# Kernel optimization log

Hardware: AMD Instinct MI355X
Metric: run time of the kernel (lower is better)

Reference implementation:

```python
import jax, jax.numpy as jnp
import numpy as np

B, Q, K, QS, KS, H, DV = 16, 128, 512, 256, 256, 128, 256


def setup_inputs() -> dict:
    key = jax.random.key(0)
    ks = jax.random.split(key, 7)
    return {
        "queries": jax.random.normal(ks[0], (B, Q, QS), dtype=jnp.float32),
        "keys": jax.random.normal(ks[1], (B, K, KS), dtype=jnp.float32),
        "values": jax.random.normal(ks[2], (B, K, DV), dtype=jnp.float32),
        "valid_lens": jax.random.randint(ks[3], (B,), 1, K + 1),
        # Linear weights (no bias); stored as [in, hidden] so x @ W == nn.Linear
        "W_q": jax.random.normal(ks[4], (QS, H), dtype=jnp.float32) / np.float32(np.sqrt(QS)),
        "W_k": jax.random.normal(ks[5], (KS, H), dtype=jnp.float32) / np.float32(np.sqrt(KS)),
        "w_v": jax.random.normal(ks[6], (H,), dtype=jnp.float32) / np.float32(np.sqrt(H)),
    }


def reference(queries, keys, values, valid_lens, W_q, W_k, w_v):
    # Projections
    q = jnp.einsum('bqd,dh->bqh', queries, W_q)   # [B,Q,H]
    k = jnp.einsum('bkd,dh->bkh', keys, W_k)      # [B,K,H]
    # Additive (Bahdanau) score: tanh(q + k) . w_v  -> [B,Q,K]
    feats = jnp.tanh(q[:, :, None, :] + k[:, None, :, :])  # [B,Q,K,H] big intermediate
    scores = jnp.einsum('bqkh,h->bqk', feats, w_v)
    # masked softmax over keys: positions >= valid_len get -1e6 (as in torch ref)
    mask = jnp.arange(K)[None, None, :] < valid_lens[:, None, None]  # [B,1,K] bcast
    scores = jnp.where(mask, scores, jnp.float32(-1e6))
    attn = jax.nn.softmax(scores, axis=-1)        # [B,Q,K]
    # dropout p=0.0 -> identity
    return jnp.einsum('bqk,bkd->bqd', attn, values)  # [B,Q,DV]
```

## Files before the change

### kernel.cpp

```cpp
#include <hip/hip_runtime.h>
#include <hip/hip_bf16.h>

#define NB 16
#define NQ 128
#define NK 512
#define DIN 256
#define NH 128
#define NDV 256

#define CSC 2.8853900817779268f

__global__ __launch_bounds__(256) void proj_both_kernel(
    const float* __restrict__ Q, const float* __restrict__ K,
    const float* __restrict__ Wq, const float* __restrict__ Wk,
    float* __restrict__ QP, float* __restrict__ KPT)
{
    __shared__ float Xl[32 * DIN];
    const int tid = threadIdx.x;
    int blk = blockIdx.x;
    const float* X; const float* W;
    int b, r0, isq;
    if (blk < 64) { isq = 1; b = blk >> 2; r0 = (blk & 3) * 32;
                    X = Q + ((size_t)b * NQ + r0) * DIN; W = Wq; }
    else { blk -= 64; isq = 0; b = blk >> 4; r0 = (blk & 15) * 32;
           X = K + ((size_t)b * NK + r0) * DIN; W = Wk; }

    {
        const float4* Xg = (const float4*)X;
        float4* Xs = (float4*)Xl;
        #pragma unroll
        for (int i = 0; i < 8; ++i) Xs[tid + 256 * i] = Xg[tid + 256 * i];
    }
    __syncthreads();

    const int h4 = tid & 31;
    const int rg = tid >> 5;
    const float4* Wv = (const float4*)W;

    float4 acc[4];
    #pragma unroll
    for (int r = 0; r < 4; ++r) { acc[r].x = 0.f; acc[r].y = 0.f; acc[r].z = 0.f; acc[r].w = 0.f; }

    float4 w0 = Wv[0 * 32 + h4], w1 = Wv[1 * 32 + h4], w2 = Wv[2 * 32 + h4], w3 = Wv[3 * 32 + h4];
    float4 n0 = Wv[4 * 32 + h4], n1 = Wv[5 * 32 + h4], n2 = Wv[6 * 32 + h4], n3 = Wv[7 * 32 + h4];
    for (int d = 0; d < DIN; d += 4) {
        const int dp = (d + 8 < DIN) ? d + 8 : 0;
        float4 m0 = Wv[(dp + 0) * 32 + h4];
        float4 m1 = Wv[(dp + 1) * 32 + h4];
        float4 m2 = Wv[(dp + 2) * 32 + h4];
        float4 m3 = Wv[(dp + 3) * 32 + h4];
        #pragma unroll
        for (int r = 0; r < 4; ++r) {
            float4 x = *(const float4*)&Xl[(rg * 4 + r) * DIN + d];
            acc[r].x += x.x * w0.x + x.y * w1.x + x.z * w2.x + x.w * w3.x;
            acc[r].y += x.x * w0.y + x.y * w1.y + x.z * w2.y + x.w * w3.y;
            acc[r].z += x.x * w0.z + x.y * w1.z + x.z * w2.z + x.w * w3.z;
            acc[r].w += x.x * w0.w + x.y * w1.w + x.z * w2.w + x.w * w3.w;
        }
        w0 = n0; w1 = n1; w2 = n2; w3 = n3;
        n0 = m0; n1 = m1; n2 = m2; n3 = m3;
    }
    #pragma unroll
    for (int r = 0; r < 4; ++r) {
        acc[r].x *= CSC; acc[r].y *= CSC; acc[r].z *= CSC; acc[r].w *= CSC;
    }

    if (isq) {
        #pragma unroll
        for (int r = 0; r < 4; ++r)
            *(float4*)&QP[((size_t)b * NQ + r0 + rg * 4 + r) * NH + 4 * h4] = acc[r];
    } else {
        float* T = Xl;
        __syncthreads();
        #pragma unroll
        for (int r = 0; r < 4; ++r) {
            T[(4 * h4 + 0) * 36 + rg * 4 + r] = acc[r].x;
            T[(4 * h4 + 1) * 36 + rg * 4 + r] = acc[r].y;
            T[(4 * h4 + 2) * 36 + rg * 4 + r] = acc[r].z;
            T[(4 * h4 + 3) * 36 + rg * 4 + r] = acc[r].w;
        }
        __syncthreads();
        #pragma unroll
        for (int i = 0; i < 4; ++i) {
            const int idx = tid + 256 * i;
            const int h = idx >> 3, c8 = idx & 7;
            float4 v = *(const float4*)&T[h * 36 + c8 * 4];
            *(float4*)&KPT[((size_t)b * NH + h) * NK + r0 + c8 * 4] = v;
        }
    }
}

__global__ __launch_bounds__(512) void attn_fused_kernel(
    const float* __restrict__ QP, const float* __restrict__ KPT,
    const float* __restrict__ wv, const int* __restrict__ vlen,
    const float* __restrict__ V, float* __restrict__ OUT)
{
    __shared__ float qcl[4 * NH];
    __shared__ float wvl[NH];
    __shared__ float sc[4][NK];
    __shared__ float part[4][4][NDV];
    const int tid = threadIdx.x;
    const int b  = blockIdx.x & 15;
    const int q0 = (blockIdx.x >> 4) * 4;

    qcl[tid] = QP[((size_t)b * NQ + q0) * NH + tid];
    if (tid < NH) wvl[tid] = -2.0f * wv[tid];
    __syncthreads();

    int vl = vlen[b];
    vl = vl < 1 ? 1 : (vl > NK ? NK : vl);

    {
        const float* kb = KPT + (size_t)b * NH * NK + tid;
        float a0 = 0.f, a1 = 0.f, a2 = 0.f, a3 = 0.f;
        #pragma unroll 4
        for (int h = 0; h < NH; ++h) {
            float kv = kb[(size_t)h * NK];
            float wq = wvl[h];
            float e0 = __builtin_amdgcn_exp2f(qcl[0 * NH + h] + kv);
            float e1 = __builtin_amdgcn_exp2f(qcl[1 * NH + h] + kv);
            float e2 = __builtin_amdgcn_exp2f(qcl[2 * NH + h] + kv);
            float e3 = __builtin_amdgcn_exp2f(qcl[3 * NH + h] + kv);
            a0 += wq * __builtin_amdgcn_rcpf(e0 + 1.0f);
            a1 += wq * __builtin_amdgcn_rcpf(e1 + 1.0f);
            a2 += wq * __builtin_amdgcn_rcpf(e2 + 1.0f);
            a3 += wq * __builtin_amdgcn_rcpf(e3 + 1.0f);
        }
        const bool vld = (tid < vl);
        sc[0][tid] = vld ? a0 : -1e6f;
        sc[1][tid] = vld ? a1 : -1e6f;
        sc[2][tid] = vld ? a2 : -1e6f;
        sc[3][tid] = vld ? a3 : -1e6f;
    }
    __syncthreads();

    const int w = tid >> 6, lane = tid & 63;
    if (w < 4) {
        float vals[8];
        float m = -3.0e38f;
        #pragma unroll
        for (int i = 0; i < 8; ++i) { vals[i] = sc[w][lane + 64 * i]; m = fmaxf(m, vals[i]); }
        #pragma unroll
        for (int off = 32; off; off >>= 1) m = fmaxf(m, __shfl_xor(m, off, 64));
        float s = 0.f;
        #pragma unroll
        for (int i = 0; i < 8; ++i) {
            vals[i] = __builtin_amdgcn_exp2f((vals[i] - m) * 1.4426950408889634f);
            s += vals[i];
        }
        #pragma unroll
        for (int off = 32; off; off >>= 1) s += __shfl_xor(s, off, 64);
        const float invs = 1.0f / s;
        #pragma unroll
        for (int i = 0; i < 8; ++i) sc[w][lane + 64 * i] = vals[i] * invs;
    }
    __syncthreads();

    float4 o[4];
    #pragma unroll
    for (int r = 0; r < 4; ++r) { o[r].x = 0.f; o[r].y = 0.f; o[r].z = 0.f; o[r].w = 0.f; }
    {
        const float* vb = V + (size_t)b * NK * NDV + lane * 4;
        const int kb0 = w * 64;
        #pragma unroll 4
        for (int kk = 0; kk < 64; ++kk) {
            const int k = kb0 + kk;
            float4 v4 = *(const float4*)(vb + (size_t)k * NDV);
            float p0 = sc[0][k], p1 = sc[1][k], p2 = sc[2][k], p3 = sc[3][k];
            o[0].x += p0 * v4.x; o[0].y += p0 * v4.y; o[0].z += p0 * v4.z; o[0].w += p0 * v4.w;
            o[1].x += p1 * v4.x; o[1].y += p1 * v4.y; o[1].z += p1 * v4.z; o[1].w += p1 * v4.w;
            o[2].x += p2 * v4.x; o[2].y += p2 * v4.y; o[2].z += p2 * v4.z; o[2].w += p2 * v4.w;
            o[3].x += p3 * v4.x; o[3].y += p3 * v4.y; o[3].z += p3 * v4.z; o[3].w += p3 * v4.w;
        }
    }
    if (w >= 4) {
        #pragma unroll
        for (int r = 0; r < 4; ++r) *(float4*)&part[w - 4][r][lane * 4] = o[r];
    }
    __syncthreads();
    if (w < 4) {
        #pragma unroll
        for (int r = 0; r < 4; ++r) {
            float4 t = *(const float4*)&part[w][r][lane * 4];
            o[r].x += t.x; o[r].y += t.y; o[r].z += t.z; o[r].w += t.w;
            *(float4*)&part[w][r][lane * 4] = o[r];
        }
    }
    __syncthreads();
    if (tid < 256) {
        const int r = tid >> 6, d4 = tid & 63;
        float4 s = {0.f, 0.f, 0.f, 0.f};
        #pragma unroll
        for (int p = 0; p < 4; ++p) {
            float4 q = *(const float4*)&part[p][r][d4 * 4];
            s.x += q.x; s.y += q.y; s.z += q.z; s.w += q.w;
        }
        *(float4*)&OUT[((size_t)b * NQ + q0 + r) * NDV + d4 * 4] = s;
    }
}

extern "C" void kernel_launch(void* const* d_in, const int* in_sizes, int n_in,
                              void* d_out, int out_size, void* d_ws, size_t ws_size,
                              hipStream_t stream) {
    const float* queries = (const float*)d_in[0];
    const float* keys    = (const float*)d_in[1];
    const float* values  = (const float*)d_in[2];
    const int*   vlen    = (const int*)d_in[3];
    const float* Wq      = (const float*)d_in[4];
    const float* Wk      = (const float*)d_in[5];
    const float* wv      = (const float*)d_in[6];
    float* out           = (float*)d_out;

    float* qp  = (float*)d_ws;
    float* kpt = qp + (size_t)NB * NQ * NH;

    proj_both_kernel<<<64 + 256, 256, 0, stream>>>(queries, keys, Wq, Wk, qp, kpt);
    attn_fused_kernel<<<NB * 32, 512, 0, stream>>>(qp, kpt, wv, vlen, values, out);
}
```

Measured before the change: 132.1 us.

## Factor tanh exponent into per-row exp products and skip masked keys

The projection kernel now stores exp2(c*q) and exp2(c*k) rather than the scaled projections. The inner score loop therefore computes 1/(eq*ek+1) with one FMA and one reciprocal, dropping the per-element exp. Key projection blocks, score computation and value accumulation are also skipped for keys beyond valid_len, and q values are stored interleaved for float4 LDS reads. Risks include overflow or underflow of the separate exponentials for large projections, which could turn into inf*0 NaNs, and skipping padded keys relies on masked weights being exactly zero after softmax.

```diff
diff --git a/kernel.cpp b/kernel.cpp
--- a/kernel.cpp
+++ b/kernel.cpp
@@ -13,7 +13,8 @@
 __global__ __launch_bounds__(256) void proj_both_kernel(
     const float* __restrict__ Q, const float* __restrict__ K,
     const float* __restrict__ Wq, const float* __restrict__ Wk,
-    float* __restrict__ QP, float* __restrict__ KPT)
+    const int* __restrict__ vlen,
+    float* __restrict__ EQ, float* __restrict__ EKT)
 {
     __shared__ float Xl[32 * DIN];
     const int tid = threadIdx.x;
@@ -23,7 +24,10 @@
     if (blk < 64) { isq = 1; b = blk >> 2; r0 = (blk & 3) * 32;
                     X = Q + ((size_t)b * NQ + r0) * DIN; W = Wq; }
     else { blk -= 64; isq = 0; b = blk >> 4; r0 = (blk & 15) * 32;
-           X = K + ((size_t)b * NK + r0) * DIN; W = Wk; }
+           X = K + ((size_t)b * NK + r0) * DIN; W = Wk;
+           int vl = vlen[b]; vl = vl < 1 ? 1 : (vl > NK ? NK : vl);
+           if (r0 >= vl) return;
+    }
 
     {
         const float4* Xg = (const float4*)X;
@@ -62,13 +66,16 @@
     }
     #pragma unroll
     for (int r = 0; r < 4; ++r) {
-        acc[r].x *= CSC; acc[r].y *= CSC; acc[r].z *= CSC; acc[r].w *= CSC;
+        acc[r].x = __builtin_amdgcn_exp2f(CSC * acc[r].x);
+        acc[r].y = __builtin_amdgcn_exp2f(CSC * acc[r].y);
+        acc[r].z = __builtin_amdgcn_exp2f(CSC * acc[r].z);
+        acc[r].w = __builtin_amdgcn_exp2f(CSC * acc[r].w);
     }
 
     if (isq) {
         #pragma unroll
         for (int r = 0; r < 4; ++r)
-            *(float4*)&QP[((size_t)b * NQ + r0 + rg * 4 + r) * NH + 4 * h4] = acc[r];
+            *(float4*)&EQ[((size_t)b * NQ + r0 + rg * 4 + r) * NH + 4 * h4] = acc[r];
     } else {
         float* T = Xl;
         __syncthreads();
@@ -85,17 +92,17 @@
             const int idx = tid + 256 * i;
             const int h = idx >> 3, c8 = idx & 7;
             float4 v = *(const float4*)&T[h * 36 + c8 * 4];
-            *(float4*)&KPT[((size_t)b * NH + h) * NK + r0 + c8 * 4] = v;
+            *(float4*)&EKT[((size_t)b * NH + h) * NK + r0 + c8 * 4] = v;
         }
     }
 }
 
 __global__ __launch_bounds__(512) void attn_fused_kernel(
-    const float* __restrict__ QP, const float* __restrict__ KPT,
+    const float* __restrict__ EQ, const float* __restrict__ EKT,
     const float* __restrict__ wv, const int* __restrict__ vlen,
     const float* __restrict__ V, float* __restrict__ OUT)
 {
-    __shared__ float qcl[4 * NH];
+    __shared__ float eq4[NH * 4];
     __shared__ float wvl[NH];
     __shared__ float sc[4][NK];
     __shared__ float part[4][4][NDV];
@@ -103,7 +110,10 @@
     const int b  = blockIdx.x & 15;
     const int q0 = (blockIdx.x >> 4) * 4;
 
-    qcl[tid] = QP[((size_t)b * NQ + q0) * NH + tid];
+    {
+        const int r = tid >> 7, h = tid & 127;
+        eq4[h * 4 + r] = EQ[((size_t)b * NQ + q0 + r) * NH + h];
+    }
     if (tid < NH) wvl[tid] = -2.0f * wv[tid];
     __syncthreads();
 
@@ -111,22 +121,21 @@
     vl = vl < 1 ? 1 : (vl > NK ? NK : vl);
 
     {
-        const float* kb = KPT + (size_t)b * NH * NK + tid;
         float a0 = 0.f, a1 = 0.f, a2 = 0.f, a3 = 0.f;
-        #pragma unroll 4
-        for (int h = 0; h < NH; ++h) {
-            float kv = kb[(size_t)h * NK];
-            float wq = wvl[h];
-            float e0 = __builtin_amdgcn_exp2f(qcl[0 * NH + h] + kv);
-            float e1 = __builtin_amdgcn_exp2f(qcl[1 * NH + h] + kv);
-            float e2 = __builtin_amdgcn_exp2f(qcl[2 * NH + h] + kv);
-            float e3 = __builtin_amdgcn_exp2f(qcl[3 * NH + h] + kv);
-            a0 += wq * __builtin_amdgcn_rcpf(e0 + 1.0f);
-            a1 += wq * __builtin_amdgcn_rcpf(e1 + 1.0f);
-            a2 += wq * __builtin_amdgcn_rcpf(e2 + 1.0f);
-            a3 += wq * __builtin_amdgcn_rcpf(e3 + 1.0f);
-        }
         const bool vld = (tid < vl);
+        if (vld) {
+            const float* kb = EKT + (size_t)b * NH * NK + tid;
+            #pragma unroll 8
+            for (int h = 0; h < NH; ++h) {
+                float ek = kb[(size_t)h * NK];
+                float4 eq = *(const float4*)&eq4[h * 4];
+                float wq = wvl[h];
+                a0 += wq * __builtin_amdgcn_rcpf(__builtin_fmaf(eq.x, ek, 1.0f));
+                a1 += wq * __builtin_amdgcn_rcpf(__builtin_fmaf(eq.y, ek, 1.0f));
+                a2 += wq * __builtin_amdgcn_rcpf(__builtin_fmaf(eq.z, ek, 1.0f));
+                a3 += wq * __builtin_amdgcn_rcpf(__builtin_fmaf(eq.w, ek, 1.0f));
+            }
+        }
         sc[0][tid] = vld ? a0 : -1e6f;
         sc[1][tid] = vld ? a1 : -1e6f;
         sc[2][tid] = vld ? a2 : -1e6f;
@@ -160,17 +169,19 @@
     #pragma unroll
     for (int r = 0; r < 4; ++r) { o[r].x = 0.f; o[r].y = 0.f; o[r].z = 0.f; o[r].w = 0.f; }
     {
-        const float* vb = V + (size_t)b * NK * NDV + lane * 4;
         const int kb0 = w * 64;
-        #pragma unroll 4
-        for (int kk = 0; kk < 64; ++kk) {
-            const int k = kb0 + kk;
-            float4 v4 = *(const float4*)(vb + (size_t)k * NDV);
-            float p0 = sc[0][k], p1 = sc[1][k], p2 = sc[2][k], p3 = sc[3][k];
-            o[0].x += p0 * v4.x; o[0].y += p0 * v4.y; o[0].z += p0 * v4.z; o[0].w += p0 * v4.w;
-            o[1].x += p1 * v4.x; o[1].y += p1 * v4.y; o[1].z += p1 * v4.z; o[1].w += p1 * v4.w;
-            o[2].x += p2 * v4.x; o[2].y += p2 * v4.y; o[2].z += p2 * v4.z; o[2].w += p2 * v4.w;
-            o[3].x += p3 * v4.x; o[3].y += p3 * v4.y; o[3].z += p3 * v4.z; o[3].w += p3 * v4.w;
+        if (kb0 < vl) {
+            const float* vb = V + (size_t)b * NK * NDV + lane * 4;
+            #pragma unroll 4
+            for (int kk = 0; kk < 64; ++kk) {
+                const int k = kb0 + kk;
+                float4 v4 = *(const float4*)(vb + (size_t)k * NDV);
+                float p0 = sc[0][k], p1 = sc[1][k], p2 = sc[2][k], p3 = sc[3][k];
+                o[0].x += p0 * v4.x; o[0].y += p0 * v4.y; o[0].z += p0 * v4.z; o[0].w += p0 * v4.w;
+                o[1].x += p1 * v4.x; o[1].y += p1 * v4.y; o[1].z += p1 * v4.z; o[1].w += p1 * v4.w;
+                o[2].x += p2 * v4.x; o[2].y += p2 * v4.y; o[2].z += p2 * v4.z; o[2].w += p2 * v4.w;
+                o[3].x += p3 * v4.x; o[3].y += p3 * v4.y; o[3].z += p3 * v4.z; o[3].w += p3 * v4.w;
+            }
         }
     }
     if (w >= 4) {
@@ -211,9 +222,9 @@
     const float* wv      = (const float*)d_in[6];
     float* out           = (float*)d_out;
 
-    float* qp  = (float*)d_ws;
-    float* kpt = qp + (size_t)NB * NQ * NH;
-
-    proj_both_kernel<<<64 + 256, 256, 0, stream>>>(queries, keys, Wq, Wk, qp, kpt);
-    attn_fused_kernel<<<NB * 32, 512, 0, stream>>>(qp, kpt, wv, vlen, values, out);
+    float* eq  = (float*)d_ws;
+    float* ekt = eq + (size_t)NB * NQ * NH;
+
+    proj_both_kernel<<<64 + 256, 256, 0, stream>>>(queries, keys, Wq, Wk, vlen, eq, ekt);
+    attn_fused_kernel<<<NB * 32, 512, 0, stream>>>(eq, ekt, wv, vlen, values, out);
 }
```

After: 143.1 us. +8.3%, slower.
